# Optimization experiments

Hardware: AMD Instinct MI355X
Metric: run time of the kernel (lower is better)

## Reference

```python
import jax, jax.numpy as jnp
import numpy as np

B, T, D, H, F = 4, 2048, 1024, 16, 4096
HD = D // H
EPS = 1e-5


def setup_inputs() -> dict:
    key = jax.random.key(0)
    ks = jax.random.split(key, 10)
    s = lambda fan_in: 1.0 / np.sqrt(fan_in)
    return {
        "x": jax.random.normal(ks[0], (B, T, D), jnp.float32),
        "ln1_g": jnp.ones((D,), jnp.float32),
        "ln1_b": jnp.zeros((D,), jnp.float32),
        "ln2_g": jnp.ones((D,), jnp.float32),
        "ln2_b": jnp.zeros((D,), jnp.float32),
        "Wq": jax.random.normal(ks[1], (H, D, HD), jnp.float32) * s(D),
        "Wk": jax.random.normal(ks[2], (H, D, HD), jnp.float32) * s(D),
        "Wv": jax.random.normal(ks[3], (H, D, HD), jnp.float32) * s(D),
        "Wo": jax.random.normal(ks[4], (D, D), jnp.float32) * s(D),
        "bo": jnp.zeros((D,), jnp.float32),
        "W1": jax.random.normal(ks[5], (D, F), jnp.float32) * s(D),
        "b1": jnp.zeros((F,), jnp.float32),
        "W2": jax.random.normal(ks[6], (F, D), jnp.float32) * s(F),
        "b2": jnp.zeros((D,), jnp.float32),
    }


def _layernorm(x, g, b):
    mu = jnp.mean(x, axis=-1, keepdims=True)
    var = jnp.mean(jnp.square(x - mu), axis=-1, keepdims=True)
    return (x - mu) * jax.lax.rsqrt(var + EPS) * g + b


def reference(x, ln1_g, ln1_b, ln2_g, ln2_b, Wq, Wk, Wv, Wo, bo, W1, b1, W2, b2):
    Bc, Tc, Dc = x.shape
    xn = _layernorm(x, ln1_g, ln1_b)
    # per-head projections (source loops over heads; here batched over h)
    q = jnp.einsum('btd,hdk->bhtk', xn, Wq)
    k = jnp.einsum('btd,hdk->bhtk', xn, Wk)
    v = jnp.einsum('btd,hdk->bhtk', xn, Wv)
    scale = jnp.asarray(Dc, x.dtype) ** -0.5  # C**-0.5 with C = embedding_dim
    scores = jnp.einsum('bhtk,bhsk->bhts', q, k) * scale
    causal = jnp.tril(jnp.ones((Tc, Tc), bool))
    scores = jnp.where(causal, scores, -jnp.inf)
    attn = jax.nn.softmax(scores, axis=-1)
    out = jnp.einsum('bhts,bhsk->bhtk', attn, v)
    out = out.transpose(0, 2, 1, 3).reshape(Bc, Tc, Dc)  # concat heads
    attn_out = out @ Wo + bo
    h = attn_out + x  # residual 1
    hn = _layernorm(h, ln2_g, ln2_b)
    ff = jax.nn.relu(hn @ W1 + b1) @ W2 + b2
    return ff + h  # residual 2
```

## Files before the change

kernel.cpp:

```cpp
#include <hip/hip_runtime.h>
#include <hip/hip_bf16.h>

#define NB 4
#define NT 2048
#define ND 1024
#define NH 16
#define NHD 64
#define NF 4096
#define MTOK (NB*NT)

typedef float f32x4 __attribute__((ext_vector_type(4)));
typedef __bf16 bf16x8 __attribute__((ext_vector_type(8)));
typedef short s16x8 __attribute__((ext_vector_type(8)));
typedef unsigned short ushort_t;

__device__ inline ushort_t f2bf(float f) {
    unsigned int u = __builtin_bit_cast(unsigned int, f);
    unsigned int r = (u + 0x7FFFu + ((u >> 16) & 1u)) >> 16;
    return (ushort_t)r;
}
__device__ inline float bf2f(ushort_t u) {
    return __builtin_bit_cast(float, (unsigned int)u << 16);
}

__device__ __forceinline__ void async_load16(const void* g, void* l) {
    __builtin_amdgcn_global_load_lds(
        (const __attribute__((address_space(1))) void*)g,
        (__attribute__((address_space(3))) void*)l, 16, 0, 0);
}

__device__ __forceinline__ unsigned int cvt_pk_bf16(float lo, float hi) {
    unsigned int r;
    asm("v_cvt_pk_bf16_f32 %0, %1, %2" : "=v"(r) : "v"(lo), "v"(hi));
    return r;
}

__device__ __forceinline__ float exp2_fast(float x) {
    float r;
    asm("v_exp_f32 %0, %1" : "=v"(r) : "v"(x));
    return r;
}

__global__ __launch_bounds__(256)
void transpose_to_bf16(const float* __restrict__ src, ushort_t* __restrict__ dst,
                       int R, int C) {
    __shared__ float tile[32][33];
    int c0 = blockIdx.x * 32, r0 = blockIdx.y * 32;
    #pragma unroll
    for (int i = 0; i < 32; i += 8)
        tile[threadIdx.y + i][threadIdx.x] =
            src[(size_t)(r0 + threadIdx.y + i) * C + c0 + threadIdx.x];
    __syncthreads();
    #pragma unroll
    for (int i = 0; i < 32; i += 8)
        dst[(size_t)(c0 + threadIdx.y + i) * R + r0 + threadIdx.x] =
            f2bf(tile[threadIdx.x][threadIdx.y + i]);
}

__global__ __launch_bounds__(256)
void transpose_qkv_to_bf16(const float* __restrict__ Wq, const float* __restrict__ Wk,
                           const float* __restrict__ Wv, ushort_t* __restrict__ dst) {
    __shared__ float tile[32][33];
    int z = blockIdx.z;
    int w = z >> 4, h = z & 15;
    const float* src = (w == 0 ? Wq : (w == 1 ? Wk : Wv)) + (size_t)h * ND * NHD;
    const float sc = (w == 0) ? 0.03125f * 1.44269504f : 1.0f;
    ushort_t* out = dst + ((size_t)w * ND + h * NHD) * ND;
    int c0 = blockIdx.x * 32, r0 = blockIdx.y * 32;
    #pragma unroll
    for (int i = 0; i < 32; i += 8)
        tile[threadIdx.y + i][threadIdx.x] =
            src[(size_t)(r0 + threadIdx.y + i) * NHD + c0 + threadIdx.x];
    __syncthreads();
    #pragma unroll
    for (int i = 0; i < 32; i += 8)
        out[(size_t)(c0 + threadIdx.y + i) * ND + r0 + threadIdx.x] =
            f2bf(tile[threadIdx.x][threadIdx.y + i] * sc);
}

__global__ __launch_bounds__(256)
void layernorm_to_bf16(const float* __restrict__ x, const float* __restrict__ g,
                       const float* __restrict__ bvec, ushort_t* __restrict__ out) {
    int row = blockIdx.x;
    const float4* xr = (const float4*)(x + (size_t)row * ND);
    float4 v = xr[threadIdx.x];
    float s = v.x + v.y + v.z + v.w;
    float s2 = v.x * v.x + v.y * v.y + v.z * v.z + v.w * v.w;
    #pragma unroll
    for (int o = 32; o >= 1; o >>= 1) {
        s += __shfl_xor(s, o);
        s2 += __shfl_xor(s2, o);
    }
    __shared__ float red[8];
    int wave = threadIdx.x >> 6, lane = threadIdx.x & 63;
    if (lane == 0) { red[wave] = s; red[4 + wave] = s2; }
    __syncthreads();
    float ts = red[0] + red[1] + red[2] + red[3];
    float ts2 = red[4] + red[5] + red[6] + red[7];
    float mu = ts * (1.f / ND);
    float var = ts2 * (1.f / ND) - mu * mu;
    float rs = rsqrtf(var + 1e-5f);
    float4 gv = ((const float4*)g)[threadIdx.x];
    float4 bv = ((const float4*)bvec)[threadIdx.x];
    ushort4 o4;
    o4.x = f2bf((v.x - mu) * rs * gv.x + bv.x);
    o4.y = f2bf((v.y - mu) * rs * gv.y + bv.y);
    o4.z = f2bf((v.z - mu) * rs * gv.z + bv.z);
    o4.w = f2bf((v.w - mu) * rs * gv.w + bv.w);
    ((ushort4*)(out + (size_t)row * ND))[threadIdx.x] = o4;
}

__global__ __launch_bounds__(256)
void layernorm_bf16(const ushort_t* __restrict__ x, const float* __restrict__ g,
                    const float* __restrict__ bvec, ushort_t* __restrict__ out) {
    int row = blockIdx.x;
    ushort4 u4 = ((const ushort4*)(x + (size_t)row * ND))[threadIdx.x];
    float4 v;
    v.x = bf2f(u4.x); v.y = bf2f(u4.y); v.z = bf2f(u4.z); v.w = bf2f(u4.w);
    float s = v.x + v.y + v.z + v.w;
    float s2 = v.x * v.x + v.y * v.y + v.z * v.z + v.w * v.w;
    #pragma unroll
    for (int o = 32; o >= 1; o >>= 1) {
        s += __shfl_xor(s, o);
        s2 += __shfl_xor(s2, o);
    }
    __shared__ float red[8];
    int wave = threadIdx.x >> 6, lane = threadIdx.x & 63;
    if (lane == 0) { red[wave] = s; red[4 + wave] = s2; }
    __syncthreads();
    float ts = red[0] + red[1] + red[2] + red[3];
    float ts2 = red[4] + red[5] + red[6] + red[7];
    float mu = ts * (1.f / ND);
    float var = ts2 * (1.f / ND) - mu * mu;
    float rs = rsqrtf(var + 1e-5f);
    float4 gv = ((const float4*)g)[threadIdx.x];
    float4 bv = ((const float4*)bvec)[threadIdx.x];
    ushort4 o4;
    o4.x = f2bf((v.x - mu) * rs * gv.x + bv.x);
    o4.y = f2bf((v.y - mu) * rs * gv.y + bv.y);
    o4.z = f2bf((v.z - mu) * rs * gv.z + bv.z);
    o4.w = f2bf((v.w - mu) * rs * gv.w + bv.w);
    ((ushort4*)(out + (size_t)row * ND))[threadIdx.x] = o4;
}

template<int BN, bool HAS_BIAS, bool RELU, int RES_MODE, bool OUT_F32>
__global__ __launch_bounds__(512, 2)
void gemm8p(const ushort_t* __restrict__ A, const ushort_t* __restrict__ Bt,
            const float* __restrict__ bias, const void* __restrict__ res,
            void* __restrict__ outp, int M, int N, int K) {
    constexpr int NFR = BN / 64;
    __shared__ __align__(16) ushort_t As[2][256 * 64];
    __shared__ __align__(16) ushort_t Bs[2][BN * 64];
    const int t = threadIdx.x;
    const int wave = t >> 6, lane = t & 63;
    const int wm = wave >> 2, wn = wave & 3;
    const int g = lane >> 4, l16 = lane & 15;
    int wid = blockIdx.y * gridDim.x + blockIdx.x;
    const int cpx = (gridDim.x * gridDim.y) >> 3;
    wid = (wid & 7) * cpx + (wid >> 3);
    const int m0 = (wid / gridDim.x) * 256;
    const int n0 = (wid % gridDim.x) * BN;
    const int lrow8 = lane >> 3;
    const int srcCol = ((lane & 7) ^ lrow8) * 8;
    const ushort_t* Abase = A + (size_t)m0 * K + srcCol;
    const ushort_t* Bbase = Bt + (size_t)n0 * K + srcCol;
    const int NKT = K >> 6;

    f32x4 acc[8][NFR] = {};

    auto stageAhalf = [&](int kt, int h, int slot) {
        #pragma unroll
        for (int j = 2 * h; j < 2 * h + 2; j++) {
            const int rowbase = j * 64 + wave * 8;
            async_load16(Abase + (size_t)(rowbase + lrow8) * K + kt * 64,
                         &As[slot][rowbase * 64]);
        }
    };
    auto stageBhalf = [&](int kt, int h, int slot) {
        if constexpr (BN == 256) {
            #pragma unroll
            for (int j = 2 * h; j < 2 * h + 2; j++) {
                const int rowbase = j * 64 + wave * 8;
                async_load16(Bbase + (size_t)(rowbase + lrow8) * K + kt * 64,
                             &Bs[slot][rowbase * 64]);
            }
        } else {
            const int rowbase = h * 64 + wave * 8;
            async_load16(Bbase + (size_t)(rowbase + lrow8) * K + kt * 64,
                         &Bs[slot][rowbase * 64]);
        }
    };

    stageAhalf(0, 0, 0); stageAhalf(0, 1, 0);
    stageBhalf(0, 0, 0); stageBhalf(0, 1, 0);
    stageBhalf(1, 0, 1); stageBhalf(1, 1, 1);
    stageAhalf(1, 0, 1);
    if constexpr (BN == 256) asm volatile("s_waitcnt vmcnt(6)" ::: "memory");
    else                     asm volatile("s_waitcnt vmcnt(4)" ::: "memory");
    __builtin_amdgcn_s_barrier();
    __builtin_amdgcn_sched_barrier(0);

    for (int kt = 0; kt < NKT; ++kt) {
        const int cur = kt & 1, nxt = cur ^ 1;
        const ushort_t* as = As[cur];
        const ushort_t* bs = Bs[cur];
        bf16x8 bfr[NFR][2];

        if constexpr (BN == 128) {
            #pragma unroll
            for (int ph = 0; ph < 2; ph++) {
                if (ph == 0) {
                    #pragma unroll
                    for (int nf = 0; nf < NFR; nf++)
                        #pragma unroll
                        for (int ks = 0; ks < 2; ks++) {
                            const int row = wn * (BN / 4) + nf * 16 + l16;
                            int a = row * 128 + ks * 64 + 16 * g;
                            a ^= (row & 7) << 4;
                            bfr[nf][ks] = *(const bf16x8*)((const char*)bs + a);
                        }
                }
                bf16x8 af[2][2][2];
                #pragma unroll
                for (int qq = 0; qq < 2; qq++)
                    #pragma unroll
                    for (int mi2 = 0; mi2 < 2; mi2++)
                        #pragma unroll
                        for (int ks = 0; ks < 2; ks++) {
                            const int row = (ph * 2 + qq) * 64 + wm * 32 + mi2 * 16 + l16;
                            int a = row * 128 + ks * 64 + 16 * g;
                            a ^= (row & 7) << 4;
                            af[qq][mi2][ks] = *(const bf16x8*)((const char*)as + a);
                        }
                if (ph == 0) {
                    if (kt + 1 < NKT) stageAhalf(kt + 1, 1, nxt);
                } else {
                    if (kt + 2 < NKT) {
                        stageBhalf(kt + 2, 0, cur);
                        stageBhalf(kt + 2, 1, cur);
                        stageAhalf(kt + 2, 0, cur);
                    }
                }
                __builtin_amdgcn_sched_barrier(0);
                if (ph == 1) {
                    if (kt >= NKT - 2) asm volatile("s_waitcnt vmcnt(0)" ::: "memory");
                    else               asm volatile("s_waitcnt vmcnt(4)" ::: "memory");
                }
                __builtin_amdgcn_s_barrier();
                __builtin_amdgcn_sched_barrier(0);
                __builtin_amdgcn_s_setprio(1);
                #pragma unroll
                for (int qq = 0; qq < 2; qq++)
                    #pragma unroll
                    for (int mi2 = 0; mi2 < 2; mi2++)
                        #pragma unroll
                        for (int nf = 0; nf < NFR; nf++)
                            #pragma unroll
                            for (int ks = 0; ks < 2; ks++)
                                acc[(ph * 2 + qq) * 2 + mi2][nf] =
                                    __builtin_amdgcn_mfma_f32_16x16x32_bf16(
                                        af[qq][mi2][ks], bfr[nf][ks],
                                        acc[(ph * 2 + qq) * 2 + mi2][nf], 0, 0, 0);
                __builtin_amdgcn_s_setprio(0);
                __builtin_amdgcn_s_barrier();
                __builtin_amdgcn_sched_barrier(0);
            }
        } else {
            #pragma unroll
            for (int q = 0; q < 4; q++) {
                if (q == 0) {
                    #pragma unroll
                    for (int nf = 0; nf < NFR; nf++)
                        #pragma unroll
                        for (int ks = 0; ks < 2; ks++) {
                            const int row = wn * (BN / 4) + nf * 16 + l16;
                            int a = row * 128 + ks * 64 + 16 * g;
                            a ^= (row & 7) << 4;
                            bfr[nf][ks] = *(const bf16x8*)((const char*)bs + a);
                        }
                }
                bf16x8 af[2][2];
                #pragma unroll
                for (int mi2 = 0; mi2 < 2; mi2++)
                    #pragma unroll
                    for (int ks = 0; ks < 2; ks++) {
                        const int row = q * 64 + wm * 32 + mi2 * 16 + l16;
                        int a = row * 128 + ks * 64 + 16 * g;
                        a ^= (row & 7) << 4;
                        af[mi2][ks] = *(const bf16x8*)((const char*)as + a);
                    }
                if (q == 0)      { if (kt + 1 < NKT) stageAhalf(kt + 1, 1, nxt); }
                else if (q == 1) { if (kt + 2 < NKT) stageBhalf(kt + 2, 0, cur); }
                else if (q == 2) { if (kt + 2 < NKT) stageBhalf(kt + 2, 1, cur); }
                else             { if (kt + 2 < NKT) stageAhalf(kt + 2, 0, cur); }
                __builtin_amdgcn_sched_barrier(0);
                if (q == 3) {
                    if (kt >= NKT - 2) asm volatile("s_waitcnt vmcnt(0)" ::: "memory");
                    else               asm volatile("s_waitcnt vmcnt(6)" ::: "memory");
                }
                __builtin_amdgcn_s_barrier();
                __builtin_amdgcn_sched_barrier(0);
                __builtin_amdgcn_s_setprio(1);
                #pragma unroll
                for (int mi2 = 0; mi2 < 2; mi2++)
                    #pragma unroll
                    for (int nf = 0; nf < NFR; nf++)
                        #pragma unroll
                        for (int ks = 0; ks < 2; ks++)
                            acc[q * 2 + mi2][nf] = __builtin_amdgcn_mfma_f32_16x16x32_bf16(
                                af[mi2][ks], bfr[nf][ks], acc[q * 2 + mi2][nf], 0, 0, 0);
                __builtin_amdgcn_s_setprio(0);
                __builtin_amdgcn_s_barrier();
                __builtin_amdgcn_sched_barrier(0);
            }
        }
    }

    const int gc0 = n0 + wn * (BN / 4) + l16;
    #pragma unroll
    for (int mi = 0; mi < 8; mi++) {
        const int rowb = m0 + (mi >> 1) * 64 + wm * 32 + (mi & 1) * 16 + g * 4;
        #pragma unroll
        for (int nf = 0; nf < NFR; nf++) {
            const int col = gc0 + nf * 16;
            float bb = 0.f;
            if constexpr (HAS_BIAS) bb = bias[col];
            #pragma unroll
            for (int r = 0; r < 4; r++) {
                const int row = rowb + r;
                float v = acc[mi][nf][r] + bb;
                if constexpr (RELU) v = fmaxf(v, 0.f);
                if constexpr (RES_MODE == 1)
                    v += ((const float*)res)[(size_t)row * N + col];
                else if constexpr (RES_MODE == 2)
                    v += bf2f(((const ushort_t*)res)[(size_t)row * N + col]);
                if constexpr (OUT_F32)
                    ((float*)outp)[(size_t)row * N + col] = v;
                else
                    ((ushort_t*)outp)[(size_t)row * N + col] = f2bf(v);
            }
        }
    }
}

template<bool HAS_BIAS, bool RELU, int RES_MODE, bool OUT_F32>
__global__ __launch_bounds__(256, 2)
void gemm2b64(const ushort_t* __restrict__ A, const ushort_t* __restrict__ Bt,
              const float* __restrict__ bias, const void* __restrict__ res,
              void* __restrict__ outp, int M, int N, int K) {
    __shared__ __align__(16) ushort_t As[2][128 * 64];
    __shared__ __align__(16) ushort_t Bs[2][128 * 64];
    const int t = threadIdx.x;
    const int wave = t >> 6, lane = t & 63;
    const int wm = wave >> 1, wn = wave & 1;
    const int g = lane >> 4, l16 = lane & 15;
    int wid = blockIdx.y * gridDim.x + blockIdx.x;
    const int cpx = (gridDim.x * gridDim.y) >> 3;
    wid = (wid & 7) * cpx + (wid >> 3);
    const int m0 = (wid / gridDim.x) * 128;
    const int n0 = (wid % gridDim.x) * 128;
    const int rw = lane >> 3, ck = lane & 7;
    const int srcCol = (ck ^ rw) * 8;
    const ushort_t* Abase = A + (size_t)m0 * K + srcCol;
    const ushort_t* Bbase = Bt + (size_t)n0 * K + srcCol;
    const int NKT = K >> 6;

    f32x4 acc[4][4] = {};

    auto stage = [&](int kt, int slot) {
        #pragma unroll
        for (int j = 0; j < 4; j++) {
            const int rowbase = j * 32 + wave * 8;
            async_load16(Abase + (size_t)(rowbase + rw) * K + kt * 64,
                         &As[slot][rowbase * 64]);
        }
        #pragma unroll
        for (int j = 0; j < 4; j++) {
            const int rowbase = j * 32 + wave * 8;
            async_load16(Bbase + (size_t)(rowbase + rw) * K + kt * 64,
                         &Bs[slot][rowbase * 64]);
        }
    };

    stage(0, 0);
    stage(1, 1);

    for (int kt = 0; kt < NKT; ++kt) {
        const int cur = kt & 1;
        if (kt >= NKT - 1) asm volatile("s_waitcnt vmcnt(0)" ::: "memory");
        else               asm volatile("s_waitcnt vmcnt(8)" ::: "memory");
        __builtin_amdgcn_s_barrier();
        __builtin_amdgcn_sched_barrier(0);

        const ushort_t* as = As[cur];
        const ushort_t* bs = Bs[cur];
        bf16x8 af[4][2], bfr[4][2];
        #pragma unroll
        for (int mi = 0; mi < 4; mi++)
            #pragma unroll
            for (int ks = 0; ks < 2; ks++) {
                const int row = wm * 64 + mi * 16 + l16;
                int a = row * 128 + ks * 64 + 16 * g;
                a ^= (row & 7) << 4;
                af[mi][ks] = *(const bf16x8*)((const char*)as + a);
            }
        #pragma unroll
        for (int nf = 0; nf < 4; nf++)
            #pragma unroll
            for (int ks = 0; ks < 2; ks++) {
                const int row = wn * 64 + nf * 16 + l16;
                int a = row * 128 + ks * 64 + 16 * g;
                a ^= (row & 7) << 4;
                bfr[nf][ks] = *(const bf16x8*)((const char*)bs + a);
            }
        __builtin_amdgcn_s_setprio(1);
        #pragma unroll
        for (int mi = 0; mi < 4; mi++)
            #pragma unroll
            for (int nf = 0; nf < 4; nf++)
                #pragma unroll
                for (int ks = 0; ks < 2; ks++)
                    acc[mi][nf] = __builtin_amdgcn_mfma_f32_16x16x32_bf16(
                        af[mi][ks], bfr[nf][ks], acc[mi][nf], 0, 0, 0);
        __builtin_amdgcn_s_setprio(0);
        __builtin_amdgcn_s_barrier();
        __builtin_amdgcn_sched_barrier(0);
        if (kt + 2 < NKT) stage(kt + 2, cur);
    }

    const int gc0 = n0 + wn * 64 + l16;
    #pragma unroll
    for (int mi = 0; mi < 4; mi++) {
        const int rowb = m0 + wm * 64 + mi * 16 + g * 4;
        #pragma unroll
        for (int nf = 0; nf < 4; nf++) {
            const int col = gc0 + nf * 16;
            float bb = 0.f;
            if constexpr (HAS_BIAS) bb = bias[col];
            #pragma unroll
            for (int r = 0; r < 4; r++) {
                const int row = rowb + r;
                float v = acc[mi][nf][r] + bb;
                if constexpr (RELU) v = fmaxf(v, 0.f);
                if constexpr (RES_MODE == 1)
                    v += ((const float*)res)[(size_t)row * N + col];
                else if constexpr (RES_MODE == 2)
                    v += bf2f(((const ushort_t*)res)[(size_t)row * N + col]);
                if constexpr (OUT_F32)
                    ((float*)outp)[(size_t)row * N + col] = v;
                else
                    ((ushort_t*)outp)[(size_t)row * N + col] = f2bf(v);
            }
        }
    }
}

__global__ __launch_bounds__(256)
void attn_kernel(const ushort_t* __restrict__ qkv, ushort_t* __restrict__ out) {
    __shared__ __align__(16) ushort_t Ks[2][64 * 64];
    __shared__ __align__(16) ushort_t Vt[2][64 * 64];
    __shared__ unsigned int Pw[4][32][35];
    const int L = blockIdx.y * gridDim.x + blockIdx.x;
    const int xcd = L & 7, kk = L >> 3;
    const int bh = ((kk & 7) << 3) | xcd;
    const int pairIdx = kk >> 3;
    const int b = bh >> 4, h = bh & 15;
    const int t = threadIdx.x, wave = t >> 6, lane = t & 63;
    const int g = lane >> 4, q16 = lane & 15;
    const size_t base = ((size_t)b * NT) * 3072 + h * NHD;
    const ushort_t* qp_base = qkv + base;
    const ushort_t* kb = qkv + base + 1024;
    const ushort_t* vb = qkv + base + 2048;
    const int krw = lane >> 3, kck = lane & 7;
    const int ksrc = (kck ^ krw) * 8;
    const int vkp = t >> 3, vdg = t & 7;

    bf16x8 ones_f;
    {
        uint4 u = {0x3F803F80u, 0x3F803F80u, 0x3F803F80u, 0x3F803F80u};
        ones_f = __builtin_bit_cast(bf16x8, u);
    }

    auto stageK = [&](int kv, int buf) {
        #pragma unroll
        for (int c = 0; c < 2; c++) {
            const int rowbase = c * 32 + wave * 8;
            async_load16(kb + (size_t)(kv * 64 + rowbase + krw) * 3072 + ksrc,
                         &Ks[buf][rowbase * 64]);
        }
    };
    auto loadV = [&](int kv, s16x8& v0, s16x8& v1) {
        const ushort_t* vp = vb + (size_t)(kv * 64 + 2 * vkp) * 3072 + vdg * 8;
        v0 = *(const s16x8*)vp;
        v1 = *(const s16x8*)(vp + 3072);
    };
    auto writeV = [&](int buf, const s16x8& v0, const s16x8& v1) {
        const uint4 w0 = __builtin_bit_cast(uint4, v0);
        const uint4 w1 = __builtin_bit_cast(uint4, v1);
        const unsigned int lw0[4] = {w0.x, w0.y, w0.z, w0.w};
        const unsigned int lw1[4] = {w1.x, w1.y, w1.z, w1.w};
        #pragma unroll
        for (int j = 0; j < 4; j++) {
            unsigned int we = __builtin_amdgcn_perm(lw1[j], lw0[j], 0x05040100u);
            unsigned int wo = __builtin_amdgcn_perm(lw1[j], lw0[j], 0x07060302u);
            int d0 = vdg * 8 + 2 * j;
            int a0 = (d0 << 7) + (vkp << 2);
            a0 ^= ((((d0) & 7) ^ (((d0) >> 3) & 7)) << 4);
            *(unsigned int*)((char*)&Vt[buf][0] + a0) = we;
            int d1 = d0 + 1;
            int a1 = (d1 << 7) + (vkp << 2);
            a1 ^= ((((d1) & 7) ^ (((d1) >> 3) & 7)) << 4);
            *(unsigned int*)((char*)&Vt[buf][0] + a1) = wo;
        }
    };

    for (int half = 0; half < 2; half++) {
        const int qt = half ? (15 - pairIdx) : pairIdx;
        const int q0 = qt * 128;
        const int wq0 = q0 + wave * 32;
        bf16x8 qf[2][2];
        #pragma unroll
        for (int qb2 = 0; qb2 < 2; qb2++) {
            const ushort_t* qp = qp_base + (size_t)(wq0 + 16 * qb2 + q16) * 3072 + 8 * g;
            qf[qb2][0] = *(const bf16x8*)qp;
            qf[qb2][1] = *(const bf16x8*)(qp + 32);
        }
        f32x4 of[2][4] = {};
        f32x4 of4[2] = {};
        const int nkv = 2 * qt + 2;

        {
            s16x8 pv0, pv1;
            stageK(0, 0);
            loadV(0, pv0, pv1);
            asm volatile("s_waitcnt vmcnt(0)" ::: "memory");
            writeV(0, pv0, pv1);
        }
        __syncthreads();

        for (int kv = 0; kv < nkv; ++kv) {
            const int cur = kv & 1, nxt = cur ^ 1;
            s16x8 pv0, pv1;
            const bool pre = (kv + 1 < nkv);
            if (pre) {
                stageK(kv + 1, nxt);
                loadV(kv + 1, pv0, pv1);
            }
            __builtin_amdgcn_sched_barrier(0);

            const int kbase = kv * 64;
            if (kbase <= wq0 + 31) {
                bf16x8 kf[4][2];
                #pragma unroll
                for (int n = 0; n < 4; n++)
                    #pragma unroll
                    for (int kd = 0; kd < 2; kd++) {
                        int row = n * 16 + q16;
                        int a = row * 128 + (kd * 64 + 16 * g);
                        a ^= ((row & 7) << 4);
                        kf[n][kd] = *(const bf16x8*)((const char*)&Ks[cur][0] + a);
                    }

                f32x4 sf[2][4] = {};
                #pragma unroll
                for (int n = 0; n < 4; n++)
                    #pragma unroll
                    for (int kd = 0; kd < 2; kd++) {
                        sf[0][n] = __builtin_amdgcn_mfma_f32_16x16x32_bf16(
                            kf[n][kd], qf[0][kd], sf[0][n], 0, 0, 0);
                        sf[1][n] = __builtin_amdgcn_mfma_f32_16x16x32_bf16(
                            kf[n][kd], qf[1][kd], sf[1][n], 0, 0, 0);
                    }

                #pragma unroll
                for (int qb2 = 0; qb2 < 2; qb2++) {
                    const int wqb = wq0 + 16 * qb2 + q16;
                    const bool partial = (kbase + 63 > wq0 + 16 * qb2);
                    float p[4][4];
                    #pragma unroll
                    for (int n = 0; n < 4; n++)
                        #pragma unroll
                        for (int r = 0; r < 4; r++) {
                            float v = sf[qb2][n][r];
                            if (partial) {
                                int kg = kbase + n * 16 + 4 * g + r;
                                if (kg > wqb) v = -1.0e30f;
                            }
                            p[n][r] = exp2_fast(v);
                        }
                    unsigned int* pr = &Pw[wave][16 * qb2 + q16][0];
                    #pragma unroll
                    for (int n = 0; n < 4; n++) {
                        pr[8 * n + 2 * g + 0] = cvt_pk_bf16(p[n][0], p[n][1]);
                        pr[8 * n + 2 * g + 1] = cvt_pk_bf16(p[n][2], p[n][3]);
                    }
                }

                #pragma unroll
                for (int kbk = 0; kbk < 2; kbk++) {
                    bf16x8 pfr[2];
                    #pragma unroll
                    for (int qb2 = 0; qb2 < 2; qb2++) {
                        const unsigned int* pr = &Pw[wave][16 * qb2 + q16][0];
                        uint4 pu;
                        pu.x = pr[16 * kbk + 4 * g + 0];
                        pu.y = pr[16 * kbk + 4 * g + 1];
                        pu.z = pr[16 * kbk + 4 * g + 2];
                        pu.w = pr[16 * kbk + 4 * g + 3];
                        pfr[qb2] = __builtin_bit_cast(bf16x8, pu);
                    }
                    of4[0] = __builtin_amdgcn_mfma_f32_16x16x32_bf16(
                        ones_f, pfr[0], of4[0], 0, 0, 0);
                    of4[1] = __builtin_amdgcn_mfma_f32_16x16x32_bf16(
                        ones_f, pfr[1], of4[1], 0, 0, 0);
                    #pragma unroll
                    for (int nf = 0; nf < 4; nf++) {
                        const int d = nf * 16 + q16;
                        int a = (d << 7) + (kbk * 64 + 16 * g);
                        a ^= (((d & 7) ^ ((d >> 3) & 7)) << 4);
                        bf16x8 vf = *(const bf16x8*)((const char*)&Vt[cur][0] + a);
                        of[0][nf] = __builtin_amdgcn_mfma_f32_16x16x32_bf16(
                            vf, pfr[0], of[0][nf], 0, 0, 0);
                        of[1][nf] = __builtin_amdgcn_mfma_f32_16x16x32_bf16(
                            vf, pfr[1], of[1][nf], 0, 0, 0);
                    }
                }
            }

            if (pre) writeV(nxt, pv0, pv1);
            __syncthreads();
        }

        #pragma unroll
        for (int qb2 = 0; qb2 < 2; qb2++) {
            float rl = 1.f / of4[qb2][0];
            const size_t orow = (size_t)b * NT + q0 + wave * 32 + 16 * qb2 + q16;
            #pragma unroll
            for (int nf = 0; nf < 4; nf++) {
                ushort4 o4;
                o4.x = f2bf(of[qb2][nf][0] * rl);
                o4.y = f2bf(of[qb2][nf][1] * rl);
                o4.z = f2bf(of[qb2][nf][2] * rl);
                o4.w = f2bf(of[qb2][nf][3] * rl);
                *(ushort4*)(out + orow * ND + h * NHD + nf * 16 + 4 * g) = o4;
            }
        }
    }
}

extern "C" void kernel_launch(void* const* d_in, const int* in_sizes, int n_in,
                              void* d_out, int out_size, void* d_ws, size_t ws_size,
                              hipStream_t stream) {
    const float* x     = (const float*)d_in[0];
    const float* ln1_g = (const float*)d_in[1];
    const float* ln1_b = (const float*)d_in[2];
    const float* ln2_g = (const float*)d_in[3];
    const float* ln2_b = (const float*)d_in[4];
    const float* Wq    = (const float*)d_in[5];
    const float* Wk    = (const float*)d_in[6];
    const float* Wv    = (const float*)d_in[7];
    const float* Wo    = (const float*)d_in[8];
    const float* bo    = (const float*)d_in[9];
    const float* W1    = (const float*)d_in[10];
    const float* b1    = (const float*)d_in[11];
    const float* W2    = (const float*)d_in[12];
    const float* b2    = (const float*)d_in[13];
    float* outp = (float*)d_out;

    char* w = (char*)d_ws;
    ushort_t* Wqkv_t = (ushort_t*)(w);
    ushort_t* Wo_t   = (ushort_t*)(w + 6291456);
    ushort_t* W1_t   = (ushort_t*)(w + 8388608);
    ushort_t* W2_t   = (ushort_t*)(w + 16777216);
    ushort_t* xn     = (ushort_t*)(w + 25165824);
    ushort_t* qkv    = (ushort_t*)(w + 41943040);
    ushort_t* attn_o = qkv + (size_t)MTOK * 3072;
    ushort_t* ff1    = qkv;
    ushort_t* hbuf   = (ushort_t*)(w + 41943040 + 67108864);

    dim3 tb(32, 8);
    transpose_qkv_to_bf16<<<dim3(2, 32, 48), tb, 0, stream>>>(Wq, Wk, Wv, Wqkv_t);
    transpose_to_bf16<<<dim3(32, 32), tb, 0, stream>>>(Wo, Wo_t, 1024, 1024);
    transpose_to_bf16<<<dim3(128, 32), tb, 0, stream>>>(W1, W1_t, 1024, 4096);
    transpose_to_bf16<<<dim3(32, 128), tb, 0, stream>>>(W2, W2_t, 4096, 1024);

    layernorm_to_bf16<<<MTOK, 256, 0, stream>>>(x, ln1_g, ln1_b, xn);

    gemm8p<128, false, false, 0, false><<<dim3(24, 32), 512, 0, stream>>>(
        xn, Wqkv_t, nullptr, nullptr, qkv, MTOK, 3072, 1024);

    attn_kernel<<<dim3(8, 64), 256, 0, stream>>>(qkv, attn_o);

    gemm8p<128, true, false, 1, false><<<dim3(8, 32), 512, 0, stream>>>(
        attn_o, Wo_t, bo, x, hbuf, MTOK, 1024, 1024);

    layernorm_bf16<<<MTOK, 256, 0, stream>>>(hbuf, ln2_g, ln2_b, xn);

    gemm8p<256, true, true, 0, false><<<dim3(16, 32), 512, 0, stream>>>(
        xn, W1_t, b1, nullptr, ff1, MTOK, NF, 1024);

    gemm2b64<true, false, 2, true><<<dim3(8, 64), 256, 0, stream>>>(
        ff1, W2_t, b2, hbuf, outp, MTOK, 1024, NF);
}
```

Measured before the change: 352.5 us.

## Emit transposed V from QKV GEMM epilogue and async-stage it in attention

```diff
diff --git a/kernel.cpp b/kernel.cpp
--- a/kernel.cpp
+++ b/kernel.cpp
@@ -143,11 +143,12 @@
     ((ushort4*)(out + (size_t)row * ND))[threadIdx.x] = o4;
 }
 
-template<int BN, bool HAS_BIAS, bool RELU, int RES_MODE, bool OUT_F32>
+template<int BN, bool HAS_BIAS, bool RELU, int RES_MODE, bool OUT_F32, int OUT_MODE = 0>
 __global__ __launch_bounds__(512, 2)
 void gemm8p(const ushort_t* __restrict__ A, const ushort_t* __restrict__ Bt,
             const float* __restrict__ bias, const void* __restrict__ res,
-            void* __restrict__ outp, int M, int N, int K) {
+            void* __restrict__ outp, ushort_t* __restrict__ vTp,
+            int M, int N, int K) {
     constexpr int NFR = BN / 64;
     __shared__ __align__(16) ushort_t As[2][256 * 64];
     __shared__ __align__(16) ushort_t Bs[2][BN * 64];
@@ -317,6 +318,26 @@
     }
 
     const int gc0 = n0 + wn * (BN / 4) + l16;
+    if constexpr (OUT_MODE == 1) {
+        if (n0 >= 2048) {
+            #pragma unroll
+            for (int mi = 0; mi < 8; mi++) {
+                const int rowb = m0 + (mi >> 1) * 64 + wm * 32 + (mi & 1) * 16 + g * 4;
+                const int b = rowb >> 11, tt = rowb & 2047;
+                #pragma unroll
+                for (int nf = 0; nf < NFR; nf++) {
+                    const int col = gc0 + nf * 16;
+                    ushort4 o4;
+                    o4.x = f2bf(acc[mi][nf][0]);
+                    o4.y = f2bf(acc[mi][nf][1]);
+                    o4.z = f2bf(acc[mi][nf][2]);
+                    o4.w = f2bf(acc[mi][nf][3]);
+                    *(ushort4*)(vTp + (size_t)(b * 1024 + col - 2048) * NT + tt) = o4;
+                }
+            }
+            return;
+        }
+    }
     #pragma unroll
     for (int mi = 0; mi < 8; mi++) {
         const int rowb = m0 + (mi >> 1) * 64 + wm * 32 + (mi & 1) * 16 + g * 4;
@@ -456,7 +477,8 @@
 }
 
 __global__ __launch_bounds__(256)
-void attn_kernel(const ushort_t* __restrict__ qkv, ushort_t* __restrict__ out) {
+void attn_kernel(const ushort_t* __restrict__ qkv, const ushort_t* __restrict__ vT,
+                 ushort_t* __restrict__ out) {
     __shared__ __align__(16) ushort_t Ks[2][64 * 64];
     __shared__ __align__(16) ushort_t Vt[2][64 * 64];
     __shared__ unsigned int Pw[4][32][35];
@@ -470,10 +492,9 @@
     const size_t base = ((size_t)b * NT) * 3072 + h * NHD;
     const ushort_t* qp_base = qkv + base;
     const ushort_t* kb = qkv + base + 1024;
-    const ushort_t* vb = qkv + base + 2048;
+    const ushort_t* vbt = vT + (size_t)bh * 64 * NT;
     const int krw = lane >> 3, kck = lane & 7;
     const int ksrc = (kck ^ krw) * 8;
-    const int vkp = t >> 3, vdg = t & 7;
 
     bf16x8 ones_f;
     {
@@ -489,28 +510,13 @@
                          &Ks[buf][rowbase * 64]);
         }
     };
-    auto loadV = [&](int kv, s16x8& v0, s16x8& v1) {
-        const ushort_t* vp = vb + (size_t)(kv * 64 + 2 * vkp) * 3072 + vdg * 8;
-        v0 = *(const s16x8*)vp;
-        v1 = *(const s16x8*)(vp + 3072);
-    };
-    auto writeV = [&](int buf, const s16x8& v0, const s16x8& v1) {
-        const uint4 w0 = __builtin_bit_cast(uint4, v0);
-        const uint4 w1 = __builtin_bit_cast(uint4, v1);
-        const unsigned int lw0[4] = {w0.x, w0.y, w0.z, w0.w};
-        const unsigned int lw1[4] = {w1.x, w1.y, w1.z, w1.w};
-        #pragma unroll
-        for (int j = 0; j < 4; j++) {
-            unsigned int we = __builtin_amdgcn_perm(lw1[j], lw0[j], 0x05040100u);
-            unsigned int wo = __builtin_amdgcn_perm(lw1[j], lw0[j], 0x07060302u);
-            int d0 = vdg * 8 + 2 * j;
-            int a0 = (d0 << 7) + (vkp << 2);
-            a0 ^= ((((d0) & 7) ^ (((d0) >> 3) & 7)) << 4);
-            *(unsigned int*)((char*)&Vt[buf][0] + a0) = we;
-            int d1 = d0 + 1;
-            int a1 = (d1 << 7) + (vkp << 2);
-            a1 ^= ((((d1) & 7) ^ (((d1) >> 3) & 7)) << 4);
-            *(unsigned int*)((char*)&Vt[buf][0] + a1) = wo;
+    auto stageV = [&](int kv, int buf) {
+        #pragma unroll
+        for (int c = 0; c < 2; c++) {
+            const int rowbase = c * 32 + wave * 8;
+            const int scol = ((kck ^ krw ^ ((c * 4 + wave) & 7)) * 8);
+            async_load16(vbt + (size_t)(rowbase + krw) * NT + kv * 64 + scol,
+                         &Vt[buf][rowbase * 64]);
         }
     };
 
@@ -529,22 +535,15 @@
         f32x4 of4[2] = {};
         const int nkv = 2 * qt + 2;
 
-        {
-            s16x8 pv0, pv1;
-            stageK(0, 0);
-            loadV(0, pv0, pv1);
-            asm volatile("s_waitcnt vmcnt(0)" ::: "memory");
-            writeV(0, pv0, pv1);
-        }
+        stageK(0, 0);
+        stageV(0, 0);
         __syncthreads();
 
         for (int kv = 0; kv < nkv; ++kv) {
             const int cur = kv & 1, nxt = cur ^ 1;
-            s16x8 pv0, pv1;
-            const bool pre = (kv + 1 < nkv);
-            if (pre) {
+            if (kv + 1 < nkv) {
                 stageK(kv + 1, nxt);
-                loadV(kv + 1, pv0, pv1);
+                stageV(kv + 1, nxt);
             }
             __builtin_amdgcn_sched_barrier(0);
 
@@ -627,7 +626,6 @@
                 }
             }
 
-            if (pre) writeV(nxt, pv0, pv1);
             __syncthreads();
         }
 
@@ -677,6 +675,7 @@
     ushort_t* attn_o = qkv + (size_t)MTOK * 3072;
     ushort_t* ff1    = qkv;
     ushort_t* hbuf   = (ushort_t*)(w + 41943040 + 67108864);
+    ushort_t* vT     = (ushort_t*)(w + 41943040 + 67108864 + 16777216);
 
     dim3 tb(32, 8);
     transpose_qkv_to_bf16<<<dim3(2, 32, 48), tb, 0, stream>>>(Wq, Wk, Wv, Wqkv_t);
@@ -686,18 +685,18 @@
 
     layernorm_to_bf16<<<MTOK, 256, 0, stream>>>(x, ln1_g, ln1_b, xn);
 
-    gemm8p<128, false, false, 0, false><<<dim3(24, 32), 512, 0, stream>>>(
-        xn, Wqkv_t, nullptr, nullptr, qkv, MTOK, 3072, 1024);
-
-    attn_kernel<<<dim3(8, 64), 256, 0, stream>>>(qkv, attn_o);
+    gemm8p<128, false, false, 0, false, 1><<<dim3(24, 32), 512, 0, stream>>>(
+        xn, Wqkv_t, nullptr, nullptr, qkv, vT, MTOK, 3072, 1024);
+
+    attn_kernel<<<dim3(8, 64), 256, 0, stream>>>(qkv, vT, attn_o);
 
     gemm8p<128, true, false, 1, false><<<dim3(8, 32), 512, 0, stream>>>(
-        attn_o, Wo_t, bo, x, hbuf, MTOK, 1024, 1024);
+        attn_o, Wo_t, bo, x, hbuf, nullptr, MTOK, 1024, 1024);
 
     layernorm_bf16<<<MTOK, 256, 0, stream>>>(hbuf, ln2_g, ln2_b, xn);
 
     gemm8p<256, true, true, 0, false><<<dim3(16, 32), 512, 0, stream>>>(
-        xn, W1_t, b1, nullptr, ff1, MTOK, NF, 1024);
+        xn, W1_t, b1, nullptr, ff1, nullptr, MTOK, NF, 1024);
 
     gemm2b64<true, false, 2, true><<<dim3(8, 64), 256, 0, stream>>>(
         ff1, W2_t, b2, hbuf, outp, MTOK, 1024, NF);
```

After: 353.7 us. No clear change (+0.4%).
